# Kernel optimization log

Measured on AMD Instinct MI355X. Metric: run time of the kernel, lower is better.

Reference implementation:

```python
import jax, jax.numpy as jnp
import numpy as np

N = 50000      # nodes
E = 600000     # edges
D = 128        # dim_h == num_features
G = 512        # graphs in batch
BN_EPS = 1e-5


def _w(k, shape, fan_in):
    return jax.random.normal(k, shape, jnp.float32) * np.float32(1.0 / np.sqrt(fan_in))


def setup_inputs() -> dict:
    key = jax.random.key(0)
    ks = jax.random.split(key, 16)
    return {
        "x": jax.random.normal(ks[0], (N, D), jnp.float32),
        "edge_index": jax.random.randint(ks[1], (2, E), 0, N, jnp.int64),
        "batch": jnp.sort(jax.random.randint(ks[2], (N,), 0, G, jnp.int64)),
        # GINConv 1 MLP: Linear -> BN -> ReLU -> Linear -> ReLU
        "c1_W1": _w(ks[3], (D, D), D), "c1_b1": jnp.zeros((D,), jnp.float32),
        "c1_g": jnp.ones((D,), jnp.float32), "c1_be": jnp.zeros((D,), jnp.float32),
        "c1_W2": _w(ks[4], (D, D), D), "c1_b2": jnp.zeros((D,), jnp.float32),
        # GINConv 2 MLP
        "c2_W1": _w(ks[5], (D, D), D), "c2_b1": jnp.zeros((D,), jnp.float32),
        "c2_g": jnp.ones((D,), jnp.float32), "c2_be": jnp.zeros((D,), jnp.float32),
        "c2_W2": _w(ks[6], (D, D), D), "c2_b2": jnp.zeros((D,), jnp.float32),
        # readout MLP
        "lin1_W": _w(ks[7], (4 * D, 4 * D), 4 * D), "lin1_b": jnp.zeros((4 * D,), jnp.float32),
        "lin2_W": _w(ks[8], (4 * D, 1), 4 * D), "lin2_b": jnp.zeros((1,), jnp.float32),
    }


def _gin_conv(x, src, dst, W1, b1, g, be, W2, b2):
    # sum aggregation of neighbor messages (PyG GINConv, eps=0)
    agg = jax.ops.segment_sum(x[src], dst, num_segments=x.shape[0])
    h = (agg + x) @ W1 + b1
    # BatchNorm1d, training mode (biased batch stats over nodes)
    mu = h.mean(axis=0)
    var = h.var(axis=0)
    h = jax.nn.relu(g * (h - mu) * jax.lax.rsqrt(var + BN_EPS) + be)
    return jax.nn.relu(h @ W2 + b2)


def _pool(h, batch):
    add = jax.ops.segment_sum(h, batch, num_segments=G)
    mx = jax.ops.segment_max(h, batch, num_segments=G)
    mx = jnp.where(jnp.isfinite(mx), mx, 0.0)  # empty segments -> 0
    return add, mx


def reference(x, edge_index, batch,
              c1_W1, c1_b1, c1_g, c1_be, c1_W2, c1_b2,
              c2_W1, c2_b1, c2_g, c2_be, c2_W2, c2_b2,
              lin1_W, lin1_b, lin2_W, lin2_b):
    src, dst = edge_index[0], edge_index[1]
    h1 = _gin_conv(x, src, dst, c1_W1, c1_b1, c1_g, c1_be, c1_W2, c1_b2)
    h2 = _gin_conv(h1, src, dst, c2_W1, c2_b1, c2_g, c2_be, c2_W2, c2_b2)
    a1, m1 = _pool(h1, batch)
    a2, m2 = _pool(h2, batch)
    h = jnp.concatenate([a1, a2, m1, m2], axis=1)  # [G, 4D]
    h = jax.nn.relu(h @ lin1_W + lin1_b)
    h = h @ lin2_W + lin2_b  # [G, 1]
    return jax.nn.sigmoid(h), h
```

## Files before the change

kernel.cpp:

```cpp
#include <hip/hip_runtime.h>

#define D 128
#define GNUM 512

typedef _Float16 f16;
typedef _Float16 f16x2 __attribute__((ext_vector_type(2)));
typedef _Float16 f16x8 __attribute__((ext_vector_type(8)));
typedef float f32x4 __attribute__((ext_vector_type(4)));

__global__ void deg_kernel(const int* __restrict__ ei, int* __restrict__ deg,
                           int nE) {
  int e = blockIdx.x * blockDim.x + threadIdx.x;
  if (e < nE) atomicAdd(&deg[ei[nE + e]], 1);
}

__global__ __launch_bounds__(256) void partial_kernel(
    const int* __restrict__ deg, int* __restrict__ partials, int n) {
  __shared__ int sh[256];
  const int t = threadIdx.x;
  const int i = blockIdx.x * 512 + t * 2;
  int s = 0;
  if (i < n) s += deg[i];
  if (i + 1 < n) s += deg[i + 1];
  sh[t] = s;
  __syncthreads();
#pragma unroll
  for (int off = 128; off > 0; off >>= 1) {
    if (t < off) sh[t] += sh[t + off];
    __syncthreads();
  }
  if (t == 0) partials[blockIdx.x] = sh[0];
}

__global__ __launch_bounds__(128) void scanp_kernel(
    int* __restrict__ partials, int nP, int* __restrict__ rowptr, int n,
    int nE) {
  __shared__ int sh[128];
  const int t = threadIdx.x;
  const int v = (t < nP) ? partials[t] : 0;
  sh[t] = v;
  __syncthreads();
#pragma unroll
  for (int off = 1; off < 128; off <<= 1) {
    int u = (t >= off) ? sh[t - off] : 0;
    __syncthreads();
    sh[t] += u;
    __syncthreads();
  }
  if (t < nP) partials[t] = sh[t] - v;
  if (t == 0) rowptr[n] = nE;
}

__global__ __launch_bounds__(256) void emit_kernel(
    const int* __restrict__ deg, const int* __restrict__ partials,
    int* __restrict__ rowptr, int* __restrict__ cursor, int n) {
  __shared__ int sh[256];
  const int t = threadIdx.x;
  const int i = blockIdx.x * 512 + t * 2;
  const int d0 = (i < n) ? deg[i] : 0;
  const int d1 = (i + 1 < n) ? deg[i + 1] : 0;
  const int s = d0 + d1;
  sh[t] = s;
  __syncthreads();
#pragma unroll
  for (int off = 1; off < 256; off <<= 1) {
    int u = (t >= off) ? sh[t - off] : 0;
    __syncthreads();
    sh[t] += u;
    __syncthreads();
  }
  int base = partials[blockIdx.x] + sh[t] - s;
  if (i < n) {
    rowptr[i] = base;
    cursor[i] = base;
    base += d0;
  }
  if (i + 1 < n) {
    rowptr[i + 1] = base;
    cursor[i + 1] = base;
  }
}

__global__ void fill_kernel(const int* __restrict__ ei, int* __restrict__ cursor,
                            int* __restrict__ csr, int nE) {
  int e = blockIdx.x * blockDim.x + threadIdx.x;
  if (e < nE) {
    int d = ei[nE + e];
    int pos = atomicAdd(&cursor[d], 1);
    csr[pos] = ei[e];
  }
}

__global__ __launch_bounds__(256) void prep_kernel(
    const float* __restrict__ x, f16* __restrict__ x16, int n4,
    const float* __restrict__ W0, const float* __restrict__ W1,
    const float* __restrict__ W2, const float* __restrict__ W3,
    f16* __restrict__ wt, const int* __restrict__ batch,
    int* __restrict__ gstart, int n, int nxblk) {
  const int b = blockIdx.x;
  if (b < nxblk) {
    int i = b * 256 + threadIdx.x;
    if (i < n4) {
      float4 v = ((const float4*)x)[i];
      union { f16 h[4]; uint2 u; } p;
      p.h[0] = (f16)v.x; p.h[1] = (f16)v.y;
      p.h[2] = (f16)v.z; p.h[3] = (f16)v.w;
      ((uint2*)x16)[i] = p.u;
    }
  } else if (b < nxblk + 256) {
    int idx = (b - nxblk) * 256 + threadIdx.x;
    int wsel = idx >> 14;
    int rem = idx & 16383;
    int col = rem >> 7, k = rem & 127;
    const float* W = (wsel == 0) ? W0 : (wsel == 1) ? W1
                                      : (wsel == 2) ? W2 : W3;
    wt[idx] = (f16)W[k * D + col];
  } else {
    int g = (b - nxblk - 256) * 256 + threadIdx.x;
    if (g > GNUM) return;
    if (g == GNUM) { gstart[g] = n; return; }
    int lo = 0, hi = n;
    while (lo < hi) {
      int mid = (lo + hi) >> 1;
      if (batch[mid] < g) lo = mid + 1; else hi = mid;
    }
    gstart[g] = lo;
  }
}

__global__ __launch_bounds__(256) void aggw_kernel(
    const f16* __restrict__ feat, const int* __restrict__ rowptr,
    const int* __restrict__ csr, f16* __restrict__ out, int n) {
  const int row = blockIdx.x * 4 + (threadIdx.x >> 6);
  const int l = threadIdx.x & 63;
  if (row >= n) return;
  const int c = l * 2;
  float a0, a1;
  {
    f16x2 v = *(const f16x2*)(feat + (size_t)row * D + c);
    a0 = (float)v[0]; a1 = (float)v[1];
  }
  const int beg = rowptr[row], end = rowptr[row + 1];
  int i = beg;
  for (; i + 7 < end; i += 8) {
    int s0 = csr[i],     s1 = csr[i + 1], s2 = csr[i + 2], s3 = csr[i + 3];
    int s4 = csr[i + 4], s5 = csr[i + 5], s6 = csr[i + 6], s7 = csr[i + 7];
    f16x2 v0 = *(const f16x2*)(feat + (size_t)s0 * D + c);
    f16x2 v1 = *(const f16x2*)(feat + (size_t)s1 * D + c);
    f16x2 v2 = *(const f16x2*)(feat + (size_t)s2 * D + c);
    f16x2 v3 = *(const f16x2*)(feat + (size_t)s3 * D + c);
    f16x2 v4 = *(const f16x2*)(feat + (size_t)s4 * D + c);
    f16x2 v5 = *(const f16x2*)(feat + (size_t)s5 * D + c);
    f16x2 v6 = *(const f16x2*)(feat + (size_t)s6 * D + c);
    f16x2 v7 = *(const f16x2*)(feat + (size_t)s7 * D + c);
    a0 += ((float)v0[0] + (float)v1[0]) + ((float)v2[0] + (float)v3[0]) +
          ((float)v4[0] + (float)v5[0]) + ((float)v6[0] + (float)v7[0]);
    a1 += ((float)v0[1] + (float)v1[1]) + ((float)v2[1] + (float)v3[1]) +
          ((float)v4[1] + (float)v5[1]) + ((float)v6[1] + (float)v7[1]);
  }
  for (; i + 3 < end; i += 4) {
    int s0 = csr[i], s1 = csr[i + 1], s2 = csr[i + 2], s3 = csr[i + 3];
    f16x2 v0 = *(const f16x2*)(feat + (size_t)s0 * D + c);
    f16x2 v1 = *(const f16x2*)(feat + (size_t)s1 * D + c);
    f16x2 v2 = *(const f16x2*)(feat + (size_t)s2 * D + c);
    f16x2 v3 = *(const f16x2*)(feat + (size_t)s3 * D + c);
    a0 += (float)v0[0] + (float)v1[0] + (float)v2[0] + (float)v3[0];
    a1 += (float)v0[1] + (float)v1[1] + (float)v2[1] + (float)v3[1];
  }
  for (; i < end; i++) {
    f16x2 v = *(const f16x2*)(feat + (size_t)csr[i] * D + c);
    a0 += (float)v[0];
    a1 += (float)v[1];
  }
  f16x2 o;
  o[0] = (f16)a0;
  o[1] = (f16)a1;
  *(f16x2*)(out + (size_t)row * D + c) = o;
}

template <int BN, int OUT>
__global__ __launch_bounds__(64) void gemm16_kernel(
    const f16* __restrict__ A, const float* __restrict__ ss,
    const f16* __restrict__ WT, const float* __restrict__ bias,
    f16* __restrict__ C, float* __restrict__ pstat, int n) {
  const int l = threadIdx.x;
  const int rw0 = blockIdx.x * 32;
  const int lr = l & 15;
  const int lq = l >> 4;
  const int lk = lq * 8;

  f32x4 acc[2][8];
#pragma unroll
  for (int m = 0; m < 2; m++)
#pragma unroll
    for (int nt = 0; nt < 8; nt++) acc[m][nt] = (f32x4)0.f;

#pragma unroll
  for (int s = 0; s < 4; s++) {
    const int k = s * 32 + lk;
    f16x8 af[2];
#pragma unroll
    for (int m = 0; m < 2; m++) {
      int row = rw0 + m * 16 + lr;
      f16x8 v = (f16x8)(f16)0.f;
      if (row < n) v = *(const f16x8*)(A + (size_t)row * D + k);
      if (BN) {
        float4 c0 = *(const float4*)(ss + k);
        float4 c1 = *(const float4*)(ss + k + 4);
        float4 h0 = *(const float4*)(ss + 128 + k);
        float4 h1 = *(const float4*)(ss + 128 + k + 4);
        f16x8 r;
        r[0] = (f16)fmaxf(0.f, fmaf((float)v[0], c0.x, h0.x));
        r[1] = (f16)fmaxf(0.f, fmaf((float)v[1], c0.y, h0.y));
        r[2] = (f16)fmaxf(0.f, fmaf((float)v[2], c0.z, h0.z));
        r[3] = (f16)fmaxf(0.f, fmaf((float)v[3], c0.w, h0.w));
        r[4] = (f16)fmaxf(0.f, fmaf((float)v[4], c1.x, h1.x));
        r[5] = (f16)fmaxf(0.f, fmaf((float)v[5], c1.y, h1.y));
        r[6] = (f16)fmaxf(0.f, fmaf((float)v[6], c1.z, h1.z));
        r[7] = (f16)fmaxf(0.f, fmaf((float)v[7], c1.w, h1.w));
        af[m] = r;
      } else {
        af[m] = v;
      }
    }
    f16x8 bf[8];
#pragma unroll
    for (int nt = 0; nt < 8; nt++)
      bf[nt] = *(const f16x8*)(WT + (size_t)(nt * 16 + lr) * D + k);
#pragma unroll
    for (int m = 0; m < 2; m++)
#pragma unroll
      for (int nt = 0; nt < 8; nt++)
        acc[m][nt] = __builtin_amdgcn_mfma_f32_16x16x32_f16(af[m], bf[nt],
                                                            acc[m][nt], 0, 0, 0);
  }

  if constexpr (OUT == 0) {
    float ts[8], tq[8];
#pragma unroll
    for (int nt = 0; nt < 8; nt++) { ts[nt] = 0.f; tq[nt] = 0.f; }
#pragma unroll
    for (int m = 0; m < 2; m++)
#pragma unroll
      for (int r = 0; r < 4; r++) {
        int row = rw0 + m * 16 + lq * 4 + r;
        if (row < n) {
#pragma unroll
          for (int nt = 0; nt < 8; nt++) {
            float v = acc[m][nt][r] + bias[nt * 16 + lr];
            C[(size_t)row * D + nt * 16 + lr] = (f16)v;
            ts[nt] += v;
            tq[nt] = fmaf(v, v, tq[nt]);
          }
        }
      }
#pragma unroll
    for (int nt = 0; nt < 8; nt++) {
      ts[nt] += __shfl_xor(ts[nt], 16); ts[nt] += __shfl_xor(ts[nt], 32);
      tq[nt] += __shfl_xor(tq[nt], 16); tq[nt] += __shfl_xor(tq[nt], 32);
    }
    if (l < 16) {
      float* ps = pstat + (size_t)blockIdx.x * 256;
#pragma unroll
      for (int nt = 0; nt < 8; nt++) {
        ps[nt * 16 + l] = ts[nt];
        ps[128 + nt * 16 + l] = tq[nt];
      }
    }
  } else {
#pragma unroll
    for (int m = 0; m < 2; m++)
#pragma unroll
      for (int r = 0; r < 4; r++) {
        int row = rw0 + m * 16 + lq * 4 + r;
        if (row < n) {
#pragma unroll
          for (int nt = 0; nt < 8; nt++) {
            float v = fmaxf(0.f, acc[m][nt][r] + bias[nt * 16 + lr]);
            C[(size_t)row * D + nt * 16 + lr] = (f16)v;
          }
        }
      }
  }
}

__global__ __launch_bounds__(256) void statreduce_kernel(
    const float* __restrict__ pstat, float* __restrict__ pstat2, int nB) {
  int c = threadIdx.x;
  float s = 0.f;
  for (int b = blockIdx.x; b < nB; b += 32)
    s += pstat[(size_t)b * 256 + c];
  pstat2[(size_t)blockIdx.x * 256 + c] = s;
}

__global__ void bnstats_kernel(const float* __restrict__ pstat2,
                               const float* __restrict__ g,
                               const float* __restrict__ be,
                               float* __restrict__ ss, int n) {
  int c = threadIdx.x;
  float s = 0.f, sq = 0.f;
#pragma unroll
  for (int i = 0; i < 32; i++) {
    s += pstat2[i * 256 + c];
    sq += pstat2[i * 256 + 128 + c];
  }
  float inv_n = 1.0f / (float)n;
  float mean = s * inv_n;
  float var = sq * inv_n - mean * mean;
  float scale = g[c] * rsqrtf(var + 1e-5f);
  ss[c] = scale;
  ss[128 + c] = be[c] - mean * scale;
}

__global__ __launch_bounds__(512) void poolout_kernel(
    const f16* __restrict__ h1, const f16* __restrict__ h2,
    const int* __restrict__ gstart, const float* __restrict__ W1,
    const float* __restrict__ b1, const float* __restrict__ W2,
    const float* __restrict__ b2, float* __restrict__ out) {
  __shared__ float prow[2][512];
  __shared__ float shred[8][2];
  const int t = threadIdx.x;
  const int g0 = blockIdx.x * 2;
  {
    const int sub = t >> 8;
    const int src = (t >> 7) & 1;
    const int c = t & 127;
    const f16* hp = src ? h2 : h1;
    const int r0 = gstart[g0 + sub], r1 = gstart[g0 + sub + 1];
    float s = 0.f, m = 0.f;
    int r = r0;
    for (; r + 1 < r1; r += 2) {
      float a = (float)hp[(size_t)r * D + c];
      float b = (float)hp[(size_t)(r + 1) * D + c];
      s += a + b;
      m = fmaxf(m, fmaxf(a, b));
    }
    if (r < r1) {
      float a = (float)hp[(size_t)r * D + c];
      s += a;
      m = fmaxf(m, a);
    }
    prow[sub][src * 128 + c] = s;
    prow[sub][256 + src * 128 + c] = m;
  }
  __syncthreads();
  float a00 = 0.f, a01 = 0.f, a10 = 0.f, a11 = 0.f;
  for (int k = 0; k < 512; k += 2) {
    float w0 = W1[(size_t)k * 512 + t];
    float w1 = W1[(size_t)(k + 1) * 512 + t];
    a00 = fmaf(prow[0][k], w0, a00);
    a01 = fmaf(prow[0][k + 1], w1, a01);
    a10 = fmaf(prow[1][k], w0, a10);
    a11 = fmaf(prow[1][k + 1], w1, a11);
  }
  const float bj = b1[t];
  const float w2 = W2[t];
  float acc0 = fmaxf(0.f, a00 + a01 + bj) * w2;
  float acc1 = fmaxf(0.f, a10 + a11 + bj) * w2;
  const int w = t >> 6, l = t & 63;
#pragma unroll
  for (int off = 32; off > 0; off >>= 1) {
    acc0 += __shfl_down(acc0, off);
    acc1 += __shfl_down(acc1, off);
  }
  if (l == 0) {
    shred[w][0] = acc0;
    shred[w][1] = acc1;
  }
  __syncthreads();
  if (t < 2) {
    float s = 0.f;
#pragma unroll
    for (int i = 0; i < 8; i++) s += shred[i][t];
    float h = s + b2[0];
    out[g0 + t] = 1.0f / (1.0f + expf(-h));
    out[GNUM + g0 + t] = h;
  }
}

extern "C" void kernel_launch(void* const* d_in, const int* in_sizes, int n_in,
                              void* d_out, int out_size, void* d_ws,
                              size_t ws_size, hipStream_t stream) {
  const float* x = (const float*)d_in[0];
  const int* ei = (const int*)d_in[1];
  const int* batch = (const int*)d_in[2];
  const float* c1_W1 = (const float*)d_in[3];
  const float* c1_b1 = (const float*)d_in[4];
  const float* c1_g  = (const float*)d_in[5];
  const float* c1_be = (const float*)d_in[6];
  const float* c1_W2 = (const float*)d_in[7];
  const float* c1_b2 = (const float*)d_in[8];
  const float* c2_W1 = (const float*)d_in[9];
  const float* c2_b1 = (const float*)d_in[10];
  const float* c2_g  = (const float*)d_in[11];
  const float* c2_be = (const float*)d_in[12];
  const float* c2_W2 = (const float*)d_in[13];
  const float* c2_b2 = (const float*)d_in[14];
  const float* lin1_W = (const float*)d_in[15];
  const float* lin1_b = (const float*)d_in[16];
  const float* lin2_W = (const float*)d_in[17];
  const float* lin2_b = (const float*)d_in[18];

  const int n = in_sizes[0] / D;
  const int nE = in_sizes[1] / 2;

  char* p = (char*)d_ws;
  auto take = [&](size_t bytes) {
    char* r = p;
    p += (bytes + 255) & ~(size_t)255;
    return r;
  };
  f16*   hpre   = (f16*)take((size_t)n * D * 2);
  f16*   aggt   = (f16*)take((size_t)n * D * 2);
  f16*   h1     = (f16*)take((size_t)n * D * 2);
  f16*   wt     = (f16*)take(4 * 16384 * 2);
  int*   deg    = (int*)take((size_t)n * 4);
  float* ssbuf  = (float*)take(256 * 4);
  int*   gstart = (int*)take((GNUM + 1) * 4);
  int* rowptr   = (int*)take((size_t)(n + 1) * 4);
  int* cursor   = (int*)take((size_t)(n + 1) * 4);
  int* partials = (int*)take(128 * 4);
  int* csr      = (int*)take((size_t)nE * 4);
  const int nB = (n + 31) / 32;
  float* pstat  = (float*)take((size_t)nB * 256 * 4);
  float* pstat2 = (float*)take(32 * 256 * 4);

  const int edge_grid = (nE + 255) / 256;
  const int aggw_grid = (n + 3) / 4;
  const int nP = (n + 511) / 512;
  const int n4 = n * D / 4;
  const int nxblk = (n4 + 255) / 256;
  const int prep_grid = nxblk + 256 + 3;

  hipMemsetAsync(deg, 0, (size_t)n * sizeof(int), stream);
  deg_kernel<<<edge_grid, 256, 0, stream>>>(ei, deg, nE);
  partial_kernel<<<nP, 256, 0, stream>>>(deg, partials, n);
  scanp_kernel<<<1, 128, 0, stream>>>(partials, nP, rowptr, n, nE);
  emit_kernel<<<nP, 256, 0, stream>>>(deg, partials, rowptr, cursor, n);
  fill_kernel<<<edge_grid, 256, 0, stream>>>(ei, cursor, csr, nE);
  prep_kernel<<<prep_grid, 256, 0, stream>>>(x, h1, n4, c1_W1, c1_W2, c2_W1,
                                             c2_W2, wt, batch, gstart, n,
                                             nxblk);

  aggw_kernel<<<aggw_grid, 256, 0, stream>>>(h1, rowptr, csr, aggt, n);
  gemm16_kernel<0, 0><<<nB, 64, 0, stream>>>(aggt, nullptr, wt, c1_b1, hpre,
                                             pstat, n);
  statreduce_kernel<<<32, 256, 0, stream>>>(pstat, pstat2, nB);
  bnstats_kernel<<<1, 128, 0, stream>>>(pstat2, c1_g, c1_be, ssbuf, n);
  gemm16_kernel<1, 1><<<nB, 64, 0, stream>>>(hpre, ssbuf, wt + 16384, c1_b2,
                                             h1, nullptr, n);

  aggw_kernel<<<aggw_grid, 256, 0, stream>>>(h1, rowptr, csr, aggt, n);
  gemm16_kernel<0, 0><<<nB, 64, 0, stream>>>(aggt, nullptr, wt + 32768, c2_b1,
                                             hpre, pstat, n);
  statreduce_kernel<<<32, 256, 0, stream>>>(pstat, pstat2, nB);
  bnstats_kernel<<<1, 128, 0, stream>>>(pstat2, c2_g, c2_be, ssbuf, n);
  gemm16_kernel<1, 1><<<nB, 64, 0, stream>>>(hpre, ssbuf, wt + 49152, c2_b2,
                                             aggt, nullptr, n);

  poolout_kernel<<<GNUM / 2, 512, 0, stream>>>(h1, aggt, gstart, lin1_W,
                                               lin1_b, lin2_W, lin2_b,
                                               (float*)d_out);
}
```

Baseline: 263.4 us.

## Fuse neighbor aggregation into first GEMM via shared-memory tile

Replaces the separate aggregation kernel and the first MLP GEMM with one kernel. Each 256-thread block gathers and sums neighbor features for 32 rows into LDS, then its four waves each compute a 32-column slice of the GEMM with MFMA and emit BN partial statistics. This removes the write and re-read of the aggregated feature buffer and one launch per layer. In exchange each block now has only 32 rows for the gather, so there is less parallelism in the latency-bound phase, and the BN GEMM loses its template branches.

```diff
diff --git a/kernel.cpp b/kernel.cpp
--- a/kernel.cpp
+++ b/kernel.cpp
@@ -128,61 +128,134 @@
   }
 }
 
-__global__ __launch_bounds__(256) void aggw_kernel(
+__global__ __launch_bounds__(256) void gemmfused_kernel(
     const f16* __restrict__ feat, const int* __restrict__ rowptr,
-    const int* __restrict__ csr, f16* __restrict__ out, int n) {
-  const int row = blockIdx.x * 4 + (threadIdx.x >> 6);
-  const int l = threadIdx.x & 63;
-  if (row >= n) return;
-  const int c = l * 2;
-  float a0, a1;
+    const int* __restrict__ csr, const f16* __restrict__ WT,
+    const float* __restrict__ bias, f16* __restrict__ C,
+    float* __restrict__ pstat, int n) {
+  __shared__ f16 alds[32][136];
+  const int t = threadIdx.x;
+  const int w = t >> 6;
+  const int l = t & 63;
+  const int rb = blockIdx.x * 32;
+
   {
-    f16x2 v = *(const f16x2*)(feat + (size_t)row * D + c);
-    a0 = (float)v[0]; a1 = (float)v[1];
-  }
-  const int beg = rowptr[row], end = rowptr[row + 1];
-  int i = beg;
-  for (; i + 7 < end; i += 8) {
-    int s0 = csr[i],     s1 = csr[i + 1], s2 = csr[i + 2], s3 = csr[i + 3];
-    int s4 = csr[i + 4], s5 = csr[i + 5], s6 = csr[i + 6], s7 = csr[i + 7];
-    f16x2 v0 = *(const f16x2*)(feat + (size_t)s0 * D + c);
-    f16x2 v1 = *(const f16x2*)(feat + (size_t)s1 * D + c);
-    f16x2 v2 = *(const f16x2*)(feat + (size_t)s2 * D + c);
-    f16x2 v3 = *(const f16x2*)(feat + (size_t)s3 * D + c);
-    f16x2 v4 = *(const f16x2*)(feat + (size_t)s4 * D + c);
-    f16x2 v5 = *(const f16x2*)(feat + (size_t)s5 * D + c);
-    f16x2 v6 = *(const f16x2*)(feat + (size_t)s6 * D + c);
-    f16x2 v7 = *(const f16x2*)(feat + (size_t)s7 * D + c);
-    a0 += ((float)v0[0] + (float)v1[0]) + ((float)v2[0] + (float)v3[0]) +
-          ((float)v4[0] + (float)v5[0]) + ((float)v6[0] + (float)v7[0]);
-    a1 += ((float)v0[1] + (float)v1[1]) + ((float)v2[1] + (float)v3[1]) +
-          ((float)v4[1] + (float)v5[1]) + ((float)v6[1] + (float)v7[1]);
-  }
-  for (; i + 3 < end; i += 4) {
-    int s0 = csr[i], s1 = csr[i + 1], s2 = csr[i + 2], s3 = csr[i + 3];
-    f16x2 v0 = *(const f16x2*)(feat + (size_t)s0 * D + c);
-    f16x2 v1 = *(const f16x2*)(feat + (size_t)s1 * D + c);
-    f16x2 v2 = *(const f16x2*)(feat + (size_t)s2 * D + c);
-    f16x2 v3 = *(const f16x2*)(feat + (size_t)s3 * D + c);
-    a0 += (float)v0[0] + (float)v1[0] + (float)v2[0] + (float)v3[0];
-    a1 += (float)v0[1] + (float)v1[1] + (float)v2[1] + (float)v3[1];
-  }
-  for (; i < end; i++) {
-    f16x2 v = *(const f16x2*)(feat + (size_t)csr[i] * D + c);
-    a0 += (float)v[0];
-    a1 += (float)v[1];
-  }
-  f16x2 o;
-  o[0] = (f16)a0;
-  o[1] = (f16)a1;
-  *(f16x2*)(out + (size_t)row * D + c) = o;
-}
-
-template <int BN, int OUT>
-__global__ __launch_bounds__(64) void gemm16_kernel(
+    const int c = l * 2;
+#pragma unroll 1
+    for (int rr = w * 8; rr < w * 8 + 8; rr++) {
+      const int row = rb + rr;
+      float a0 = 0.f, a1 = 0.f;
+      if (row < n) {
+        f16x2 v = *(const f16x2*)(feat + (size_t)row * D + c);
+        a0 = (float)v[0]; a1 = (float)v[1];
+        const int beg = rowptr[row], end = rowptr[row + 1];
+        int i = beg;
+        for (; i + 7 < end; i += 8) {
+          int s0 = csr[i],     s1 = csr[i + 1], s2 = csr[i + 2], s3 = csr[i + 3];
+          int s4 = csr[i + 4], s5 = csr[i + 5], s6 = csr[i + 6], s7 = csr[i + 7];
+          f16x2 v0 = *(const f16x2*)(feat + (size_t)s0 * D + c);
+          f16x2 v1 = *(const f16x2*)(feat + (size_t)s1 * D + c);
+          f16x2 v2 = *(const f16x2*)(feat + (size_t)s2 * D + c);
+          f16x2 v3 = *(const f16x2*)(feat + (size_t)s3 * D + c);
+          f16x2 v4 = *(const f16x2*)(feat + (size_t)s4 * D + c);
+          f16x2 v5 = *(const f16x2*)(feat + (size_t)s5 * D + c);
+          f16x2 v6 = *(const f16x2*)(feat + (size_t)s6 * D + c);
+          f16x2 v7 = *(const f16x2*)(feat + (size_t)s7 * D + c);
+          a0 += ((float)v0[0] + (float)v1[0]) + ((float)v2[0] + (float)v3[0]) +
+                ((float)v4[0] + (float)v5[0]) + ((float)v6[0] + (float)v7[0]);
+          a1 += ((float)v0[1] + (float)v1[1]) + ((float)v2[1] + (float)v3[1]) +
+                ((float)v4[1] + (float)v5[1]) + ((float)v6[1] + (float)v7[1]);
+        }
+        for (; i + 3 < end; i += 4) {
+          int s0 = csr[i], s1 = csr[i + 1], s2 = csr[i + 2], s3 = csr[i + 3];
+          f16x2 v0 = *(const f16x2*)(feat + (size_t)s0 * D + c);
+          f16x2 v1 = *(const f16x2*)(feat + (size_t)s1 * D + c);
+          f16x2 v2 = *(const f16x2*)(feat + (size_t)s2 * D + c);
+          f16x2 v3 = *(const f16x2*)(feat + (size_t)s3 * D + c);
+          a0 += (float)v0[0] + (float)v1[0] + (float)v2[0] + (float)v3[0];
+          a1 += (float)v0[1] + (float)v1[1] + (float)v2[1] + (float)v3[1];
+        }
+        for (; i < end; i++) {
+          f16x2 v = *(const f16x2*)(feat + (size_t)csr[i] * D + c);
+          a0 += (float)v[0];
+          a1 += (float)v[1];
+        }
+      }
+      f16x2 o;
+      o[0] = (f16)a0;
+      o[1] = (f16)a1;
+      *(f16x2*)(&alds[rr][c]) = o;
+    }
+  }
+  __syncthreads();
+
+  const int lr = l & 15;
+  const int lq = l >> 4;
+  const int lk = lq * 8;
+  const int cb = w * 32;
+
+  f32x4 acc[2][2];
+#pragma unroll
+  for (int m = 0; m < 2; m++)
+#pragma unroll
+    for (int nt = 0; nt < 2; nt++) acc[m][nt] = (f32x4)0.f;
+
+#pragma unroll
+  for (int s = 0; s < 4; s++) {
+    const int k = s * 32 + lk;
+    f16x8 af[2];
+#pragma unroll
+    for (int m = 0; m < 2; m++)
+      af[m] = *(const f16x8*)(&alds[m * 16 + lr][k]);
+    f16x8 bf[2];
+#pragma unroll
+    for (int nt = 0; nt < 2; nt++)
+      bf[nt] = *(const f16x8*)(WT + (size_t)(cb + nt * 16 + lr) * D + k);
+#pragma unroll
+    for (int m = 0; m < 2; m++)
+#pragma unroll
+      for (int nt = 0; nt < 2; nt++)
+        acc[m][nt] = __builtin_amdgcn_mfma_f32_16x16x32_f16(af[m], bf[nt],
+                                                            acc[m][nt], 0, 0, 0);
+  }
+
+  float ts[2], tq[2];
+#pragma unroll
+  for (int nt = 0; nt < 2; nt++) { ts[nt] = 0.f; tq[nt] = 0.f; }
+#pragma unroll
+  for (int m = 0; m < 2; m++)
+#pragma unroll
+    for (int r = 0; r < 4; r++) {
+      int row = rb + m * 16 + lq * 4 + r;
+      if (row < n) {
+#pragma unroll
+        for (int nt = 0; nt < 2; nt++) {
+          float v = acc[m][nt][r] + bias[cb + nt * 16 + lr];
+          C[(size_t)row * D + cb + nt * 16 + lr] = (f16)v;
+          ts[nt] += v;
+          tq[nt] = fmaf(v, v, tq[nt]);
+        }
+      }
+    }
+#pragma unroll
+  for (int nt = 0; nt < 2; nt++) {
+    ts[nt] += __shfl_xor(ts[nt], 16); ts[nt] += __shfl_xor(ts[nt], 32);
+    tq[nt] += __shfl_xor(tq[nt], 16); tq[nt] += __shfl_xor(tq[nt], 32);
+  }
+  if (l < 16) {
+    float* ps = pstat + (size_t)blockIdx.x * 256;
+#pragma unroll
+    for (int nt = 0; nt < 2; nt++) {
+      ps[cb + nt * 16 + l] = ts[nt];
+      ps[128 + cb + nt * 16 + l] = tq[nt];
+    }
+  }
+}
+
+__global__ __launch_bounds__(64) void gemmbn_kernel(
     const f16* __restrict__ A, const float* __restrict__ ss,
     const f16* __restrict__ WT, const float* __restrict__ bias,
-    f16* __restrict__ C, float* __restrict__ pstat, int n) {
+    f16* __restrict__ C, int n) {
   const int l = threadIdx.x;
   const int rw0 = blockIdx.x * 32;
   const int lr = l & 15;
@@ -198,30 +271,26 @@
 #pragma unroll
   for (int s = 0; s < 4; s++) {
     const int k = s * 32 + lk;
+    float4 c0 = *(const float4*)(ss + k);
+    float4 c1 = *(const float4*)(ss + k + 4);
+    float4 h0 = *(const float4*)(ss + 128 + k);
+    float4 h1 = *(const float4*)(ss + 128 + k + 4);
     f16x8 af[2];
 #pragma unroll
     for (int m = 0; m < 2; m++) {
       int row = rw0 + m * 16 + lr;
       f16x8 v = (f16x8)(f16)0.f;
       if (row < n) v = *(const f16x8*)(A + (size_t)row * D + k);
-      if (BN) {
-        float4 c0 = *(const float4*)(ss + k);
-        float4 c1 = *(const float4*)(ss + k + 4);
-        float4 h0 = *(const float4*)(ss + 128 + k);
-        float4 h1 = *(const float4*)(ss + 128 + k + 4);
-        f16x8 r;
-        r[0] = (f16)fmaxf(0.f, fmaf((float)v[0], c0.x, h0.x));
-        r[1] = (f16)fmaxf(0.f, fmaf((float)v[1], c0.y, h0.y));
-        r[2] = (f16)fmaxf(0.f, fmaf((float)v[2], c0.z, h0.z));
-        r[3] = (f16)fmaxf(0.f, fmaf((float)v[3], c0.w, h0.w));
-        r[4] = (f16)fmaxf(0.f, fmaf((float)v[4], c1.x, h1.x));
-        r[5] = (f16)fmaxf(0.f, fmaf((float)v[5], c1.y, h1.y));
-        r[6] = (f16)fmaxf(0.f, fmaf((float)v[6], c1.z, h1.z));
-        r[7] = (f16)fmaxf(0.f, fmaf((float)v[7], c1.w, h1.w));
-        af[m] = r;
-      } else {
-        af[m] = v;
-      }
+      f16x8 r;
+      r[0] = (f16)fmaxf(0.f, fmaf((float)v[0], c0.x, h0.x));
+      r[1] = (f16)fmaxf(0.f, fmaf((float)v[1], c0.y, h0.y));
+      r[2] = (f16)fmaxf(0.f, fmaf((float)v[2], c0.z, h0.z));
+      r[3] = (f16)fmaxf(0.f, fmaf((float)v[3], c0.w, h0.w));
+      r[4] = (f16)fmaxf(0.f, fmaf((float)v[4], c1.x, h1.x));
+      r[5] = (f16)fmaxf(0.f, fmaf((float)v[5], c1.y, h1.y));
+      r[6] = (f16)fmaxf(0.f, fmaf((float)v[6], c1.z, h1.z));
+      r[7] = (f16)fmaxf(0.f, fmaf((float)v[7], c1.w, h1.w));
+      af[m] = r;
     }
     f16x8 bf[8];
 #pragma unroll
@@ -235,53 +304,19 @@
                                                             acc[m][nt], 0, 0, 0);
   }
 
-  if constexpr (OUT == 0) {
-    float ts[8], tq[8];
-#pragma unroll
-    for (int nt = 0; nt < 8; nt++) { ts[nt] = 0.f; tq[nt] = 0.f; }
-#pragma unroll
-    for (int m = 0; m < 2; m++)
-#pragma unroll
-      for (int r = 0; r < 4; r++) {
-        int row = rw0 + m * 16 + lq * 4 + r;
-        if (row < n) {
-#pragma unroll
-          for (int nt = 0; nt < 8; nt++) {
-            float v = acc[m][nt][r] + bias[nt * 16 + lr];
-            C[(size_t)row * D + nt * 16 + lr] = (f16)v;
-            ts[nt] += v;
-            tq[nt] = fmaf(v, v, tq[nt]);
-          }
+#pragma unroll
+  for (int m = 0; m < 2; m++)
+#pragma unroll
+    for (int r = 0; r < 4; r++) {
+      int row = rw0 + m * 16 + lq * 4 + r;
+      if (row < n) {
+#pragma unroll
+        for (int nt = 0; nt < 8; nt++) {
+          float v = fmaxf(0.f, acc[m][nt][r] + bias[nt * 16 + lr]);
+          C[(size_t)row * D + nt * 16 + lr] = (f16)v;
         }
       }
-#pragma unroll
-    for (int nt = 0; nt < 8; nt++) {
-      ts[nt] += __shfl_xor(ts[nt], 16); ts[nt] += __shfl_xor(ts[nt], 32);
-      tq[nt] += __shfl_xor(tq[nt], 16); tq[nt] += __shfl_xor(tq[nt], 32);
-    }
-    if (l < 16) {
-      float* ps = pstat + (size_t)blockIdx.x * 256;
-#pragma unroll
-      for (int nt = 0; nt < 8; nt++) {
-        ps[nt * 16 + l] = ts[nt];
-        ps[128 + nt * 16 + l] = tq[nt];
-      }
-    }
-  } else {
-#pragma unroll
-    for (int m = 0; m < 2; m++)
-#pragma unroll
-      for (int r = 0; r < 4; r++) {
-        int row = rw0 + m * 16 + lq * 4 + r;
-        if (row < n) {
-#pragma unroll
-          for (int nt = 0; nt < 8; nt++) {
-            float v = fmaxf(0.f, acc[m][nt][r] + bias[nt * 16 + lr]);
-            C[(size_t)row * D + nt * 16 + lr] = (f16)v;
-          }
-        }
-      }
-  }
+    }
 }
 
 __global__ __launch_bounds__(256) void statreduce_kernel(
@@ -411,7 +446,7 @@
     return r;
   };
   f16*   hpre   = (f16*)take((size_t)n * D * 2);
-  f16*   aggt   = (f16*)take((size_t)n * D * 2);
+  f16*   h2buf  = (f16*)take((size_t)n * D * 2);
   f16*   h1     = (f16*)take((size_t)n * D * 2);
   f16*   wt     = (f16*)take(4 * 16384 * 2);
   int*   deg    = (int*)take((size_t)n * 4);
@@ -426,7 +461,6 @@
   float* pstat2 = (float*)take(32 * 256 * 4);
 
   const int edge_grid = (nE + 255) / 256;
-  const int aggw_grid = (n + 3) / 4;
   const int nP = (n + 511) / 512;
   const int n4 = n * D / 4;
   const int nxblk = (n4 + 255) / 256;
@@ -442,23 +476,20 @@
                                              c2_W2, wt, batch, gstart, n,
                                              nxblk);
 
-  aggw_kernel<<<aggw_grid, 256, 0, stream>>>(h1, rowptr, csr, aggt, n);
-  gemm16_kernel<0, 0><<<nB, 64, 0, stream>>>(aggt, nullptr, wt, c1_b1, hpre,
-                                             pstat, n);
+  gemmfused_kernel<<<nB, 256, 0, stream>>>(h1, rowptr, csr, wt, c1_b1, hpre,
+                                           pstat, n);
   statreduce_kernel<<<32, 256, 0, stream>>>(pstat, pstat2, nB);
   bnstats_kernel<<<1, 128, 0, stream>>>(pstat2, c1_g, c1_be, ssbuf, n);
-  gemm16_kernel<1, 1><<<nB, 64, 0, stream>>>(hpre, ssbuf, wt + 16384, c1_b2,
-                                             h1, nullptr, n);
-
-  aggw_kernel<<<aggw_grid, 256, 0, stream>>>(h1, rowptr, csr, aggt, n);
-  gemm16_kernel<0, 0><<<nB, 64, 0, stream>>>(aggt, nullptr, wt + 32768, c2_b1,
-                                             hpre, pstat, n);
+  gemmbn_kernel<<<nB, 64, 0, stream>>>(hpre, ssbuf, wt + 16384, c1_b2, h1, n);
+
+  gemmfused_kernel<<<nB, 256, 0, stream>>>(h1, rowptr, csr, wt + 32768, c2_b1,
+                                           hpre, pstat, n);
   statreduce_kernel<<<32, 256, 0, stream>>>(pstat, pstat2, nB);
   bnstats_kernel<<<1, 128, 0, stream>>>(pstat2, c2_g, c2_be, ssbuf, n);
-  gemm16_kernel<1, 1><<<nB, 64, 0, stream>>>(hpre, ssbuf, wt + 49152, c2_b2,
-                                             aggt, nullptr, n);
-
-  poolout_kernel<<<GNUM / 2, 512, 0, stream>>>(h1, aggt, gstart, lin1_W,
+  gemmbn_kernel<<<nB, 64, 0, stream>>>(hpre, ssbuf, wt + 49152, c2_b2,
+                                       h2buf, n);
+
+  poolout_kernel<<<GNUM / 2, 512, 0, stream>>>(h1, h2buf, gstart, lin1_W,
                                                lin1_b, lin2_W, lin2_b,
                                                (float*)d_out);
 }
```

Result: faster. 254.6 us (-3.3%).
